# Performance work log

Hardware: AMD Instinct MI355X
Metric: run time of the kernel (lower is better)

## Reference

```python
import jax, jax.numpy as jnp
import numpy as np
import math

B, T, E, HS = 8, 2048, 1024, 64  # batch, seq, n_embd, head_size (n_embd // n_head)


def setup_inputs() -> dict:
    key = jax.random.key(0)
    ks = jax.random.split(key, 7)
    sc = 1.0 / math.sqrt(E)  # roughly nn.Linear init scale
    return {
        "inputs": jax.random.normal(ks[0], (B, T, E), dtype=jnp.float32),
        "Wq": jax.random.normal(ks[1], (HS, E), dtype=jnp.float32) * sc,
        "bq": jax.random.normal(ks[2], (HS,), dtype=jnp.float32) * sc,
        "Wk": jax.random.normal(ks[3], (HS, E), dtype=jnp.float32) * sc,
        "bk": jax.random.normal(ks[4], (HS,), dtype=jnp.float32) * sc,
        "Wv": jax.random.normal(ks[5], (HS, E), dtype=jnp.float32) * sc,
        "bv": jax.random.normal(ks[6], (HS,), dtype=jnp.float32) * sc,
    }


def reference(inputs, Wq, bq, Wk, bk, Wv, bv):
    # Linear projections: x @ W.T + b  -> [B, T, HS]
    q = jnp.einsum("bte,he->bth", inputs, Wq) + bq
    k = jnp.einsum("bte,he->bth", inputs, Wk) + bk
    v = jnp.einsum("bte,he->bth", inputs, Wv) + bv

    # Scaled scores: [B, T, T]
    scores = jnp.einsum("bqh,bkh->bqk", q, k) / math.sqrt(HS)

    # Causal mask exactly as original: scores * tril - 1e12 * (1 - tril)
    tril = jnp.tril(jnp.ones((T, T), dtype=scores.dtype))
    scores = scores * tril - 1e12 * (1.0 - tril)

    attn = jax.nn.softmax(scores, axis=-1)
    # dropout p=0 (eval) -> identity
    out = jnp.einsum("bqk,bkh->bqh", attn, v)  # [B, T, HS]
    return out
```

## Files before the change

### kernel.cpp

```cpp
#include <hip/hip_runtime.h>
#include <hip/hip_bf16.h>


typedef __attribute__((ext_vector_type(8))) short short8;
typedef __attribute__((ext_vector_type(4))) float f32x4;

#if __has_builtin(__builtin_amdgcn_exp2f)
#define EXP2(x) __builtin_amdgcn_exp2f(x)
#else
#define EXP2(x) exp2f(x)
#endif

#define QSCALE 0.18033688f

__device__ inline unsigned short f2bf(float f) {
    unsigned int u = __builtin_bit_cast(unsigned int, f);
    u += 0x7FFF + ((u >> 16) & 1);
    return (unsigned short)(u >> 16);
}

__global__ __launch_bounds__(64) void prep_w(
    const float* __restrict__ Wq, const float* __restrict__ Wk,
    const float* __restrict__ Wv, unsigned short* __restrict__ Wfrag)
{
    const int ct = blockIdx.x >> 5;
    const int kk = blockIdx.x & 31;
    const int L  = threadIdx.x;
    const int l16 = L & 15, quad = L >> 4;
    const int col = ct * 16 + l16;

    const float* W; int row; float scale = 1.0f;
    if (col < 64)       { W = Wq; row = col;       scale = QSCALE; }
    else if (col < 128) { W = Wk; row = col - 64; }
    else                { W = Wv; row = col - 128; }

    const float* p = W + (size_t)row * 1024 + kk * 32 + quad * 8;
    alignas(16) unsigned short tmp[8];
    #pragma unroll
    for (int j = 0; j < 8; j++) tmp[j] = f2bf(p[j] * scale);
    unsigned short* dst = Wfrag + ((size_t)blockIdx.x * 64 + L) * 8;
    *reinterpret_cast<int4*>(dst) = *reinterpret_cast<const int4*>(tmp);
}

#define XLD 1032
__global__ __launch_bounds__(256, 4) void qkv_kernel(
    const float* __restrict__ x, const unsigned short* __restrict__ Wfrag,
    const float* __restrict__ bq, const float* __restrict__ bk,
    const float* __restrict__ bv,
    unsigned short* __restrict__ Qb, unsigned short* __restrict__ Kf,
    unsigned short* __restrict__ Vf)
{
    __shared__ alignas(16) unsigned short xs[32][XLD];

    const int tid  = threadIdx.x;
    const int m0   = blockIdx.x * 32;
    const int lane = tid & 63;
    const int w    = tid >> 6;
    const int l16  = lane & 15, quad = lane >> 4;

    #pragma unroll
    for (int i = 0; i < 16; i++) {
        int ch  = tid + 256 * i;
        int r   = ch >> 7;
        int c16 = ch & 127;
        const float* p = x + (size_t)(m0 + r) * 1024 + c16 * 8;
        float4 v0 = *reinterpret_cast<const float4*>(p);
        float4 v1 = *reinterpret_cast<const float4*>(p + 4);
        alignas(16) unsigned short t8[8] = {
            f2bf(v0.x), f2bf(v0.y), f2bf(v0.z), f2bf(v0.w),
            f2bf(v1.x), f2bf(v1.y), f2bf(v1.z), f2bf(v1.w)};
        *reinterpret_cast<int4*>(&xs[r][c16 * 8]) =
            *reinterpret_cast<const int4*>(t8);
    }
    __syncthreads();

    const int ct0 = w * 3;
    f32x4 acc[2][3];
    #pragma unroll
    for (int a = 0; a < 2; a++)
        #pragma unroll
        for (int c = 0; c < 3; c++) acc[a][c] = (f32x4){0.f, 0.f, 0.f, 0.f};

    short8 bcur[3];
    #pragma unroll
    for (int ci = 0; ci < 3; ci++)
        bcur[ci] = *reinterpret_cast<const short8*>(
            Wfrag + ((size_t)((ct0 + ci) * 32) * 64 + lane) * 8);

    for (int kk = 0; kk < 32; kk++) {
        const int kkn = (kk < 31) ? kk + 1 : 31;
        short8 bnxt[3];
        #pragma unroll
        for (int ci = 0; ci < 3; ci++)
            bnxt[ci] = *reinterpret_cast<const short8*>(
                Wfrag + ((size_t)((ct0 + ci) * 32 + kkn) * 64 + lane) * 8);

        short8 a0 = *reinterpret_cast<const short8*>(&xs[l16][kk * 32 + quad * 8]);
        short8 a1 = *reinterpret_cast<const short8*>(&xs[16 + l16][kk * 32 + quad * 8]);
        #pragma unroll
        for (int ci = 0; ci < 3; ci++) {
            acc[0][ci] = __builtin_amdgcn_mfma_f32_16x16x32_bf16(a0, bcur[ci], acc[0][ci], 0, 0, 0);
            acc[1][ci] = __builtin_amdgcn_mfma_f32_16x16x32_bf16(a1, bcur[ci], acc[1][ci], 0, 0, 0);
        }
        #pragma unroll
        for (int ci = 0; ci < 3; ci++) bcur[ci] = bnxt[ci];
    }

    const int bi = m0 >> 11;
    #pragma unroll
    for (int rt = 0; rt < 2; rt++) {
        #pragma unroll
        for (int ci = 0; ci < 3; ci++) {
            const int ct = ct0 + ci;
            const int h  = (ct & 3) * 16 + l16;
            if (ct < 4) {
                float bias = bq[h] * QSCALE;
                #pragma unroll
                for (int i = 0; i < 4; i++) {
                    size_t m = (size_t)(m0 + rt * 16 + quad * 4 + i);
                    Qb[m * 64 + h] = f2bf(acc[rt][ci][i] + bias);
                }
            } else if (ct < 8) {
                float bias = bk[h];
                #pragma unroll
                for (int i = 0; i < 4; i++) {
                    int t   = m0 + rt * 16 + quad * 4 + i;
                    int tin = t & 63;
                    int kt  = (t & 2047) >> 6;
                    int f   = ((h >> 5) << 2) | (tin >> 4);
                    int lp  = (tin & 15) | (((h >> 3) & 3) << 4);
                    Kf[(((size_t)(bi * 32 + kt) * 8 + f) * 64 + lp) * 8 + (h & 7)]
                        = f2bf(acc[rt][ci][i] + bias);
                }
            } else {
                float bias = bv[h];
                int tb  = m0 + rt * 16 + quad * 4;
                int tin = tb & 63;
                int kt  = (tb & 2047) >> 6;
                int f   = ((tin >> 5) << 2) | (h >> 4);
                int lp  = (h & 15) | (((tin >> 3) & 3) << 4);
                alignas(8) unsigned short tmp[4];
                #pragma unroll
                for (int i = 0; i < 4; i++) tmp[i] = f2bf(acc[rt][ci][i] + bias);
                unsigned short* dst =
                    Vf + (((size_t)(bi * 32 + kt) * 8 + f) * 64 + lp) * 8 + (tin & 7);
                *reinterpret_cast<int2*>(dst) = *reinterpret_cast<const int2*>(tmp);
            }
        }
    }
}

__global__ __launch_bounds__(256, 4) void attn_part(
    const unsigned short* __restrict__ Qb,
    const unsigned short* __restrict__ Kf,
    const unsigned short* __restrict__ Vf,
    float* __restrict__ Opart, float* __restrict__ Lpart)
{
    __shared__ alignas(16) unsigned short ps[4][16][72];

    const int bid = blockIdx.x;
    const int b   = bid & 7;
    const int j64 = (bid >> 3) & 31;
    const int c   = bid >> 8;
    const int nkt = j64 + 1;
    const int kt0 = c * 4;
    if (kt0 >= nkt) return;
    const int kt1 = (kt0 + 4 < nkt) ? kt0 + 4 : nkt;

    const int tid  = threadIdx.x;
    const int w    = tid >> 6;
    const int lane = tid & 63;
    const int l16  = lane & 15, quad = lane >> 4;
    const int j16  = j64 * 4 + w;
    const int q0   = j16 * 16;

    const unsigned short* qrow = Qb + ((size_t)(b * 2048 + q0 + l16)) * 64 + quad * 8;
    short8 aq0 = *reinterpret_cast<const short8*>(qrow);
    short8 aq1 = *reinterpret_cast<const short8*>(qrow + 32);

    const unsigned short* Kbat = Kf + (size_t)(b * 32) * 4096;
    const unsigned short* Vbat = Vf + (size_t)(b * 32) * 4096;

    f32x4 o[4];
    float rs = 0.f;
    #pragma unroll
    for (int i = 0; i < 4; i++) o[i] = (f32x4){0, 0, 0, 0};

    for (int kt = kt0; kt < kt1; kt++) {
        short8 kfr[8], vfr[8];
        {
            const unsigned short* kb = Kbat + (size_t)kt * 4096 + lane * 8;
            const unsigned short* vb = Vbat + (size_t)kt * 4096 + lane * 8;
            #pragma unroll
            for (int f = 0; f < 8; f++) {
                kfr[f] = *reinterpret_cast<const short8*>(kb + f * 512);
                vfr[f] = *reinterpret_cast<const short8*>(vb + f * 512);
            }
        }

        f32x4 s[4];
        #pragma unroll
        for (int ct = 0; ct < 4; ct++) s[ct] = (f32x4){0, 0, 0, 0};
        #pragma unroll
        for (int ks2 = 0; ks2 < 2; ks2++) {
            short8 aqf = ks2 ? aq1 : aq0;
            #pragma unroll
            for (int ct = 0; ct < 4; ct++)
                s[ct] = __builtin_amdgcn_mfma_f32_16x16x32_bf16(
                    kfr[ks2 * 4 + ct], aqf, s[ct], 0, 0, 0);
        }

        if (kt == nkt - 1) {
            const int qr = q0 + l16;
            #pragma unroll
            for (int ct = 0; ct < 4; ct++) {
                #pragma unroll
                for (int i = 0; i < 4; i++) {
                    int kc = kt * 64 + ct * 16 + quad * 4 + i;
                    if (kc > qr) s[ct][i] = -1e30f;
                }
            }
        }

        #pragma unroll
        for (int ct = 0; ct < 4; ct++) {
            alignas(8) unsigned short t4[4];
            #pragma unroll
            for (int i = 0; i < 4; i++) {
                float p = EXP2(s[ct][i]);
                rs += p;
                t4[i] = f2bf(p);
            }
            *reinterpret_cast<int2*>(&ps[w][l16][ct * 16 + quad * 4]) =
                *reinterpret_cast<const int2*>(t4);
        }

        short8 ap0 = *reinterpret_cast<const short8*>(&ps[w][l16][quad * 8]);
        short8 ap1 = *reinterpret_cast<const short8*>(&ps[w][l16][32 + quad * 8]);

        #pragma unroll
        for (int ks2 = 0; ks2 < 2; ks2++) {
            short8 apf = ks2 ? ap1 : ap0;
            #pragma unroll
            for (int ct = 0; ct < 4; ct++)
                o[ct] = __builtin_amdgcn_mfma_f32_16x16x32_bf16(
                    apf, vfr[ks2 * 4 + ct], o[ct], 0, 0, 0);
        }
    }

    const int pid = (c << 10) | (j16 << 3) | b;
    float* op = Opart + (size_t)pid * 1024;
    #pragma unroll
    for (int i = 0; i < 4; i++) {
        int r = quad * 4 + i;
        #pragma unroll
        for (int ct = 0; ct < 4; ct++)
            op[(size_t)r * 64 + ct * 16 + l16] = o[ct][i];
    }
    float v = rs;
    v += __shfl_xor(v, 16);
    v += __shfl_xor(v, 32);
    if (quad == 0) Lpart[(size_t)pid * 16 + l16] = v;
}

__global__ __launch_bounds__(256) void attn_combine(
    const float* __restrict__ Opart, const float* __restrict__ Lpart,
    float* __restrict__ out)
{
    const int t0 = blockIdx.x * 256 + threadIdx.x;
    #pragma unroll
    for (int it = 0; it < 2; it++) {
        const int v    = t0 + it * 131072;
        const int flat = v * 4;
        const int b    = flat >> 17;
        const int rem  = flat & 131071;
        const int t    = rem >> 6;
        const int h0   = rem & 63;
        const int j16  = t >> 4, row = t & 15;
        const int nch  = ((j16 >> 2) + 4) >> 2;
        const int pidb = (j16 << 3) | b;

        float4 acc = {0.f, 0.f, 0.f, 0.f};
        float  l   = 0.f;
        for (int c = 0; c < nch; c++) {
            const int pid = (c << 10) | pidb;
            const float* op = Opart + (size_t)pid * 1024 + row * 64 + h0;
            float4 x4 = *reinterpret_cast<const float4*>(op);
            acc.x += x4.x; acc.y += x4.y; acc.z += x4.z; acc.w += x4.w;
            l += Lpart[(size_t)pid * 16 + row];
        }
        const float inv = 1.f / l;
        float4 r = {acc.x * inv, acc.y * inv, acc.z * inv, acc.w * inv};
        *reinterpret_cast<float4*>(out + flat) = r;
    }
}

extern "C" void kernel_launch(void* const* d_in, const int* in_sizes, int n_in,
                              void* d_out, int out_size, void* d_ws, size_t ws_size,
                              hipStream_t stream) {
    const float* x  = (const float*)d_in[0];
    const float* Wq = (const float*)d_in[1];
    const float* bq = (const float*)d_in[2];
    const float* Wk = (const float*)d_in[3];
    const float* bk = (const float*)d_in[4];
    const float* Wv = (const float*)d_in[5];
    const float* bv = (const float*)d_in[6];
    float* out = (float*)d_out;

    unsigned short* Qb    = (unsigned short*)d_ws;
    unsigned short* Kf    = Qb + (size_t)16384 * 64;
    unsigned short* Vf    = Kf + (size_t)16384 * 64;
    unsigned short* Wfrag = Vf + (size_t)16384 * 64;
    float* Opart = (float*)(Wfrag + (size_t)12 * 32 * 64 * 8);
    float* Lpart = Opart + (size_t)8192 * 1024;

    prep_w<<<384, 64, 0, stream>>>(Wq, Wk, Wv, Wfrag);
    qkv_kernel<<<512, 256, 0, stream>>>(x, Wfrag, bq, bk, bv, Qb, Kf, Vf);
    attn_part<<<2048, 256, 0, stream>>>(Qb, Kf, Vf, Opart, Lpart);
    attn_combine<<<512, 256, 0, stream>>>(Opart, Lpart, out);
}
```

Measured before the change: 135.8 us.

## Pipeline x tile loads through double-buffered LDS in QKV projection

The QKV projection kernel no longer stages the whole 32x1024 bf16 x tile in LDS before computing. It now splits the K dimension into four 256-wide chunks, double-buffered in a much smaller shared array. The next chunk is prefetched into registers while MFMAs run on the current one. This overlaps global loads with compute, but adds per-stage barriers and register pressure, and lowers the launch-bounds occupancy hint from 4 to 2.

```diff
diff --git a/kernel.cpp b/kernel.cpp
--- a/kernel.cpp
+++ b/kernel.cpp
@@ -42,68 +42,111 @@
     *reinterpret_cast<int4*>(dst) = *reinterpret_cast<const int4*>(tmp);
 }
 
-#define XLD 1032
-__global__ __launch_bounds__(256, 4) void qkv_kernel(
+#define XSLD 260
+__global__ __launch_bounds__(256, 2) void qkv_kernel(
     const float* __restrict__ x, const unsigned short* __restrict__ Wfrag,
     const float* __restrict__ bq, const float* __restrict__ bk,
     const float* __restrict__ bv,
     unsigned short* __restrict__ Qb, unsigned short* __restrict__ Kf,
     unsigned short* __restrict__ Vf)
 {
-    __shared__ alignas(16) unsigned short xs[32][XLD];
+    __shared__ alignas(16) unsigned short xs[2][32][XSLD];
 
     const int tid  = threadIdx.x;
     const int m0   = blockIdx.x * 32;
     const int lane = tid & 63;
     const int w    = tid >> 6;
     const int l16  = lane & 15, quad = lane >> 4;
-
-    #pragma unroll
-    for (int i = 0; i < 16; i++) {
-        int ch  = tid + 256 * i;
-        int r   = ch >> 7;
-        int c16 = ch & 127;
-        const float* p = x + (size_t)(m0 + r) * 1024 + c16 * 8;
-        float4 v0 = *reinterpret_cast<const float4*>(p);
-        float4 v1 = *reinterpret_cast<const float4*>(p + 4);
+    const int ct0  = w * 3;
+
+    const int sr = (tid * 4) >> 5;
+    (void)sr;
+
+    float4 regs[8];
+    #pragma unroll
+    for (int i = 0; i < 4; i++) {
+        int ch = tid + 256 * i;
+        int r = ch >> 5, c8 = ch & 31;
+        const float* p = x + (size_t)(m0 + r) * 1024 + c8 * 8;
+        regs[2 * i]     = *reinterpret_cast<const float4*>(p);
+        regs[2 * i + 1] = *reinterpret_cast<const float4*>(p + 4);
+    }
+
+    f32x4 acc[2][3];
+    #pragma unroll
+    for (int a = 0; a < 2; a++)
+        #pragma unroll
+        for (int c = 0; c < 3; c++) acc[a][c] = (f32x4){0.f, 0.f, 0.f, 0.f};
+
+    short8 bcur[3];
+    #pragma unroll
+    for (int ci = 0; ci < 3; ci++)
+        bcur[ci] = *reinterpret_cast<const short8*>(
+            Wfrag + ((size_t)((ct0 + ci) * 32) * 64 + lane) * 8);
+
+    #pragma unroll
+    for (int i = 0; i < 4; i++) {
+        int ch = tid + 256 * i;
+        int r = ch >> 5, c8 = ch & 31;
+        float4 v0 = regs[2 * i], v1 = regs[2 * i + 1];
         alignas(16) unsigned short t8[8] = {
             f2bf(v0.x), f2bf(v0.y), f2bf(v0.z), f2bf(v0.w),
             f2bf(v1.x), f2bf(v1.y), f2bf(v1.z), f2bf(v1.w)};
-        *reinterpret_cast<int4*>(&xs[r][c16 * 8]) =
+        *reinterpret_cast<int4*>(&xs[0][r][c8 * 8]) =
             *reinterpret_cast<const int4*>(t8);
     }
     __syncthreads();
 
-    const int ct0 = w * 3;
-    f32x4 acc[2][3];
-    #pragma unroll
-    for (int a = 0; a < 2; a++)
-        #pragma unroll
-        for (int c = 0; c < 3; c++) acc[a][c] = (f32x4){0.f, 0.f, 0.f, 0.f};
-
-    short8 bcur[3];
-    #pragma unroll
-    for (int ci = 0; ci < 3; ci++)
-        bcur[ci] = *reinterpret_cast<const short8*>(
-            Wfrag + ((size_t)((ct0 + ci) * 32) * 64 + lane) * 8);
-
-    for (int kk = 0; kk < 32; kk++) {
-        const int kkn = (kk < 31) ? kk + 1 : 31;
-        short8 bnxt[3];
-        #pragma unroll
-        for (int ci = 0; ci < 3; ci++)
-            bnxt[ci] = *reinterpret_cast<const short8*>(
-                Wfrag + ((size_t)((ct0 + ci) * 32 + kkn) * 64 + lane) * 8);
-
-        short8 a0 = *reinterpret_cast<const short8*>(&xs[l16][kk * 32 + quad * 8]);
-        short8 a1 = *reinterpret_cast<const short8*>(&xs[16 + l16][kk * 32 + quad * 8]);
-        #pragma unroll
-        for (int ci = 0; ci < 3; ci++) {
-            acc[0][ci] = __builtin_amdgcn_mfma_f32_16x16x32_bf16(a0, bcur[ci], acc[0][ci], 0, 0, 0);
-            acc[1][ci] = __builtin_amdgcn_mfma_f32_16x16x32_bf16(a1, bcur[ci], acc[1][ci], 0, 0, 0);
-        }
-        #pragma unroll
-        for (int ci = 0; ci < 3; ci++) bcur[ci] = bnxt[ci];
+    for (int s = 0; s < 4; s++) {
+        if (s < 3) {
+            #pragma unroll
+            for (int i = 0; i < 4; i++) {
+                int ch = tid + 256 * i;
+                int r = ch >> 5, c8 = ch & 31;
+                const float* p = x + (size_t)(m0 + r) * 1024 + (s + 1) * 256 + c8 * 8;
+                regs[2 * i]     = *reinterpret_cast<const float4*>(p);
+                regs[2 * i + 1] = *reinterpret_cast<const float4*>(p + 4);
+            }
+        }
+
+        const int buf = s & 1;
+        #pragma unroll
+        for (int kk2 = 0; kk2 < 8; kk2++) {
+            const int kk  = s * 8 + kk2;
+            const int kkn = (kk < 31) ? kk + 1 : 31;
+            short8 bnxt[3];
+            #pragma unroll
+            for (int ci = 0; ci < 3; ci++)
+                bnxt[ci] = *reinterpret_cast<const short8*>(
+                    Wfrag + ((size_t)((ct0 + ci) * 32 + kkn) * 64 + lane) * 8);
+
+            short8 a0 = *reinterpret_cast<const short8*>(
+                &xs[buf][l16][kk2 * 32 + quad * 8]);
+            short8 a1 = *reinterpret_cast<const short8*>(
+                &xs[buf][16 + l16][kk2 * 32 + quad * 8]);
+            #pragma unroll
+            for (int ci = 0; ci < 3; ci++) {
+                acc[0][ci] = __builtin_amdgcn_mfma_f32_16x16x32_bf16(a0, bcur[ci], acc[0][ci], 0, 0, 0);
+                acc[1][ci] = __builtin_amdgcn_mfma_f32_16x16x32_bf16(a1, bcur[ci], acc[1][ci], 0, 0, 0);
+            }
+            #pragma unroll
+            for (int ci = 0; ci < 3; ci++) bcur[ci] = bnxt[ci];
+        }
+
+        if (s < 3) {
+            #pragma unroll
+            for (int i = 0; i < 4; i++) {
+                int ch = tid + 256 * i;
+                int r = ch >> 5, c8 = ch & 31;
+                float4 v0 = regs[2 * i], v1 = regs[2 * i + 1];
+                alignas(16) unsigned short t8[8] = {
+                    f2bf(v0.x), f2bf(v0.y), f2bf(v0.z), f2bf(v0.w),
+                    f2bf(v1.x), f2bf(v1.y), f2bf(v1.z), f2bf(v1.w)};
+                *reinterpret_cast<int4*>(&xs[buf ^ 1][r][c8 * 8]) =
+                    *reinterpret_cast<const int4*>(t8);
+            }
+            __syncthreads();
+        }
     }
 
     const int bi = m0 >> 11;
```

Result: slower. 141.2 us (+4.0%).

## Stage K/V tiles into double-buffered LDS via async global_load_lds

Applied to the files above, without the earlier changes.

Previously each of the four waves loaded the full K and V tile for a key block into registers, so every block read the tile from global memory four times. The new code has each wave issue a quarter of the tile with global_load_lds into a double-buffered shared array. The next tile is prefetched while the current one is computed, and waves then read their MFMA operands from LDS. This adds LDS pressure, a barrier per iteration, and drops the occupancy hint from launch bounds.

```diff
diff --git a/kernel.cpp b/kernel.cpp
--- a/kernel.cpp
+++ b/kernel.cpp
@@ -17,6 +17,12 @@
     unsigned int u = __builtin_bit_cast(unsigned int, f);
     u += 0x7FFF + ((u >> 16) & 1);
     return (unsigned short)(u >> 16);
+}
+
+__device__ inline void load_lds16(const void* g, void* l) {
+    __builtin_amdgcn_global_load_lds(
+        (const __attribute__((address_space(1))) void*)g,
+        (__attribute__((address_space(3))) void*)l, 16, 0, 0);
 }
 
 __global__ __launch_bounds__(64) void prep_w(
@@ -150,12 +156,13 @@
     }
 }
 
-__global__ __launch_bounds__(256, 4) void attn_part(
+__global__ __launch_bounds__(256) void attn_part(
     const unsigned short* __restrict__ Qb,
     const unsigned short* __restrict__ Kf,
     const unsigned short* __restrict__ Vf,
     float* __restrict__ Opart, float* __restrict__ Lpart)
 {
+    __shared__ alignas(16) unsigned short kv[2][16][64][8];
     __shared__ alignas(16) unsigned short ps[4][16][72];
 
     const int bid = blockIdx.x;
@@ -186,17 +193,25 @@
     #pragma unroll
     for (int i = 0; i < 4; i++) o[i] = (f32x4){0, 0, 0, 0};
 
+    #define STAGE_KT(ktv, bufv)                                             \
+        {                                                                   \
+            _Pragma("unroll")                                               \
+            for (int j = 0; j < 4; j++) {                                   \
+                int f = w * 4 + j;                                          \
+                const unsigned short* src =                                 \
+                    (f < 8 ? Kbat + (size_t)(ktv) * 4096 + f * 512          \
+                           : Vbat + (size_t)(ktv) * 4096 + (f - 8) * 512)   \
+                    + lane * 8;                                             \
+                load_lds16(src, &kv[bufv][f][0][0]);                        \
+            }                                                               \
+        }
+
+    STAGE_KT(kt0, 0);
+    __syncthreads();
+
     for (int kt = kt0; kt < kt1; kt++) {
-        short8 kfr[8], vfr[8];
-        {
-            const unsigned short* kb = Kbat + (size_t)kt * 4096 + lane * 8;
-            const unsigned short* vb = Vbat + (size_t)kt * 4096 + lane * 8;
-            #pragma unroll
-            for (int f = 0; f < 8; f++) {
-                kfr[f] = *reinterpret_cast<const short8*>(kb + f * 512);
-                vfr[f] = *reinterpret_cast<const short8*>(vb + f * 512);
-            }
-        }
+        const int buf = (kt - kt0) & 1;
+        if (kt + 1 < kt1) STAGE_KT(kt + 1, buf ^ 1);
 
         f32x4 s[4];
         #pragma unroll
@@ -205,9 +220,12 @@
         for (int ks2 = 0; ks2 < 2; ks2++) {
             short8 aqf = ks2 ? aq1 : aq0;
             #pragma unroll
-            for (int ct = 0; ct < 4; ct++)
+            for (int ct = 0; ct < 4; ct++) {
+                short8 kf8 = *reinterpret_cast<const short8*>(
+                    &kv[buf][ks2 * 4 + ct][lane][0]);
                 s[ct] = __builtin_amdgcn_mfma_f32_16x16x32_bf16(
-                    kfr[ks2 * 4 + ct], aqf, s[ct], 0, 0, 0);
+                    kf8, aqf, s[ct], 0, 0, 0);
+            }
         }
 
         if (kt == nkt - 1) {
@@ -242,10 +260,15 @@
         for (int ks2 = 0; ks2 < 2; ks2++) {
             short8 apf = ks2 ? ap1 : ap0;
             #pragma unroll
-            for (int ct = 0; ct < 4; ct++)
+            for (int ct = 0; ct < 4; ct++) {
+                short8 vf8 = *reinterpret_cast<const short8*>(
+                    &kv[buf][8 + ks2 * 4 + ct][lane][0]);
                 o[ct] = __builtin_amdgcn_mfma_f32_16x16x32_bf16(
-                    apf, vfr[ks2 * 4 + ct], o[ct], 0, 0, 0);
-        }
+                    apf, vf8, o[ct], 0, 0, 0);
+            }
+        }
+
+        if (kt + 1 < kt1) __syncthreads();
     }
 
     const int pid = (c << 10) | (j16 << 3) | b;
```

Result: no change. 134.3 us (-1.1%).
